# Kernel optimization log

Measured on AMD Instinct MI355X. Metric: run time of the kernel, lower is better.

The kernel has to match this reference:

```python
import jax, jax.numpy as jnp
import numpy as np
from jax import lax

E = 8          # num_experts
K = 2          # top-k
TASKS = 8
GATE_DIM = 16
# (in, expand, out, kernel, stride) per MoE stage
STAGES = [(3, 32, 16, 7, 2), (16, 64, 32, 3, 1), (32, 128, 64, 3, 2), (64, 256, 64, 3, 1), (64, 128, 32, 3, 1)]
DN = ('NCHW', 'OIHW', 'NCHW')


def _pw(x, w):
    return lax.conv_general_dilated(x, w, (1, 1), 'VALID', dimension_numbers=DN)


def _dw(x, w, s):
    p = w.shape[-1] // 2
    return lax.conv_general_dilated(x, w, (s, s), [(p, p), (p, p)], dimension_numbers=DN, feature_group_count=x.shape[1])


def _gn(x, scale, bias):
    # GroupNorm with num_groups = C // 4, eps = 1e-5 (torch default)
    B, C, H, W = x.shape
    G = C // 4
    xr = x.reshape(B, G, -1)
    m = xr.mean(-1, keepdims=True)
    v = xr.var(-1, keepdims=True)
    xn = ((xr - m) * lax.rsqrt(v + 1e-5)).reshape(B, C, H, W)
    return xn * scale[None, :, None, None] + bias[None, :, None, None]


def _dsc(x, p, stride):
    # DSCBlock: pw-conv -> GN -> SiLU -> dw-conv -> GN -> SiLU -> pw-conv -> GN
    w1, s1, b1, w2, s2, b2, w3, s3, b3 = p
    x = jax.nn.silu(_gn(_pw(x, w1), s1, b1))
    x = jax.nn.silu(_gn(_dw(x, w2, stride), s2, b2))
    return _gn(_pw(x, w3), s3, b3)


def _moe(gate_input, x, wg, p, stride, task_bh):
    # task-conditioned top-k softmax gating (noisy_gating=False, all aux loss weights 0)
    logits = gate_input @ wg[task_bh]                      # (B, E)
    probs = jax.nn.softmax(logits, axis=-1)
    topv, topi = lax.top_k(probs, K)
    topv = topv / topv.sum(-1, keepdims=True)              # renormalize top-k gates
    Bn = gate_input.shape[0]
    dense = jnp.zeros_like(probs).at[jnp.arange(Bn)[:, None], topi].set(topv)
    eo = jax.vmap(lambda pe: _dsc(x, pe, stride))(p)       # (E, B, C, H, W)
    return jnp.einsum('be,ebchw->bchw', dense, eo)


def _forward(fl, task_bh):
    gi, xi, ppe = fl[0], fl[1], fl[2]
    x = xi
    for i, (_, _, _, _, s) in enumerate(STAGES):
        base = 3 + i * 10
        wg = fl[base]
        p = tuple(fl[base + 1: base + 10])
        x = _moe(gi, x, wg, p, s, task_bh)
    Bn = x.shape[0]
    # patchify: (B,32,20,20) -> unfold(2,4,4).unfold(3,4,4) -> permute -> (B,25,512)
    patches = x.reshape(Bn, 32, 5, 4, 5, 4).transpose(0, 1, 2, 4, 3, 5)  # (B,32,5,5,4,4)
    patches = patches.transpose(0, 2, 3, 4, 5, 1).reshape(Bn, 25, 512)
    return patches + ppe


def setup_inputs():
    key = jax.random.key(0)
    ks = iter(jax.random.split(key, 256))
    B = 64
    d = {}
    d['gate_input'] = jax.random.normal(next(ks), (B, GATE_DIM), jnp.float32)
    d['expert_input'] = jax.random.normal(next(ks), (B, 3, 80, 80), jnp.float32)
    d['patch_pos_embed'] = 0.02 * jax.random.normal(next(ks), (1, 25, 512), jnp.float32)
    for i, (cin, exp, cout, k, s) in enumerate(STAGES, 1):
        d[f's{i}_wg'] = 0.1 * jax.random.normal(next(ks), (TASKS, GATE_DIM, E), jnp.float32)
        d[f's{i}_w1'] = jax.random.normal(next(ks), (E, exp, cin, 1, 1), jnp.float32) / np.sqrt(cin)
        d[f's{i}_g1s'] = 1.0 + 0.1 * jax.random.normal(next(ks), (E, exp), jnp.float32)
        d[f's{i}_g1b'] = 0.1 * jax.random.normal(next(ks), (E, exp), jnp.float32)
        d[f's{i}_w2'] = jax.random.normal(next(ks), (E, exp, 1, k, k), jnp.float32) / k
        d[f's{i}_g2s'] = 1.0 + 0.1 * jax.random.normal(next(ks), (E, exp), jnp.float32)
        d[f's{i}_g2b'] = 0.1 * jax.random.normal(next(ks), (E, exp), jnp.float32)
        d[f's{i}_w3'] = jax.random.normal(next(ks), (E, cout, exp, 1, 1), jnp.float32) / np.sqrt(exp)
        d[f's{i}_g3s'] = 1.0 + 0.1 * jax.random.normal(next(ks), (E, cout), jnp.float32)
        d[f's{i}_g3b'] = 0.1 * jax.random.normal(next(ks), (E, cout), jnp.float32)
    d['task_bh'] = 3
    return d


def reference(gate_input, expert_input, patch_pos_embed, s1_wg, s1_w1, s1_g1s, s1_g1b, s1_w2, s1_g2s, s1_g2b, s1_w3, s1_g3s, s1_g3b, s2_wg, s2_w1, s2_g1s, s2_g1b, s2_w2, s2_g2s, s2_g2b, s2_w3, s2_g3s, s2_g3b, s3_wg, s3_w1, s3_g1s, s3_g1b, s3_w2, s3_g2s, s3_g2b, s3_w3, s3_g3s, s3_g3b, s4_wg, s4_w1, s4_g1s, s4_g1b, s4_w2, s4_g2s, s4_g2b, s4_w3, s4_g3s, s4_g3b, s5_wg, s5_w1, s5_g1s, s5_g1b, s5_w2, s5_g2s, s5_g2b, s5_w3, s5_g3s, s5_g3b, task_bh):
    fl = (gate_input, expert_input, patch_pos_embed,
          s1_wg, s1_w1, s1_g1s, s1_g1b, s1_w2, s1_g2s, s1_g2b, s1_w3, s1_g3s, s1_g3b,
          s2_wg, s2_w1, s2_g1s, s2_g1b, s2_w2, s2_g2s, s2_g2b, s2_w3, s2_g3s, s2_g3b,
          s3_wg, s3_w1, s3_g1s, s3_g1b, s3_w2, s3_g2s, s3_g2b, s3_w3, s3_g3s, s3_g3b,
          s4_wg, s4_w1, s4_g1s, s4_g1b, s4_w2, s4_g2s, s4_g2b, s4_w3, s4_g3s, s4_g3b,
          s5_wg, s5_w1, s5_g1s, s5_g1b, s5_w2, s5_g2s, s5_g2b, s5_w3, s5_g3s, s5_g3b)
    patches = _forward(fl, task_bh)
    loss = jnp.zeros((), patches.dtype)  # all MoE loss weights are 0 in VisionEncoder
    return (patches, loss)
```

## Files before the change

kernel.cpp:

```cpp
#include <hip/hip_runtime.h>
#include <cstddef>

#define TPB 256

typedef __attribute__((ext_vector_type(8))) short short8v;
typedef __attribute__((ext_vector_type(4))) float f32x4;

__device__ __forceinline__ int rfl(int v) { return __builtin_amdgcn_readfirstlane(v); }
__device__ __forceinline__ float rflf(float v) {
    return __int_as_float(__builtin_amdgcn_readfirstlane(__float_as_int(v)));
}

__device__ __forceinline__ unsigned short f2bf(float f) {
    union { float f; unsigned int u; } x{f};
    unsigned int r = x.u + 0x7fffu + ((x.u >> 16) & 1u);
    return (unsigned short)(r >> 16);
}
__device__ __forceinline__ float bf2f(unsigned short u) {
    return __uint_as_float(((unsigned int)u) << 16);
}

template <int N, int NW>
__device__ __forceinline__ void bredN(float* v, float* red) {
    __syncthreads();
    #pragma unroll
    for (int off = 32; off > 0; off >>= 1)
        #pragma unroll
        for (int i = 0; i < N; i++) v[i] += __shfl_down(v[i], off);
    const int lane = threadIdx.x & 63;
    const int wv = threadIdx.x >> 6;
    if (lane == 0)
        #pragma unroll
        for (int i = 0; i < N; i++) red[wv * N + i] = v[i];
    __syncthreads();
    if (threadIdx.x == 0) {
        #pragma unroll
        for (int i = 0; i < N; i++) {
            float s = 0.f;
            #pragma unroll
            for (int w = 0; w < NW; w++) s += red[w * N + i];
            red[i] = s;
        }
    }
    __syncthreads();
    #pragma unroll
    for (int i = 0; i < N; i++) v[i] = red[i];
}

__device__ __forceinline__ float silu_f(float v) {
    return v * __builtin_amdgcn_rcpf(1.f + __expf(-v));
}

struct GatePtrs { const float* wg[5]; };

__global__ void gate_kernel(const float* __restrict__ gi, GatePtrs gp,
                            const int* __restrict__ taskp,
                            int* __restrict__ gidx, float* __restrict__ gw) {
    const int s = blockIdx.x;
    const int b = threadIdx.x;
    const int task = taskp[0];
    const float* wg = gp.wg[s] + (size_t)task * 16 * 8;
    float l[8];
    #pragma unroll
    for (int e = 0; e < 8; e++) l[e] = 0.f;
    for (int d = 0; d < 16; d++) {
        float v = gi[b * 16 + d];
        #pragma unroll
        for (int e = 0; e < 8; e++) l[e] += v * wg[d * 8 + e];
    }
    float mx = l[0];
    #pragma unroll
    for (int e = 1; e < 8; e++) mx = fmaxf(mx, l[e]);
    float p[8]; float sum = 0.f;
    #pragma unroll
    for (int e = 0; e < 8; e++) { p[e] = expf(l[e] - mx); sum += p[e]; }
    int i0 = 0;
    #pragma unroll
    for (int e = 1; e < 8; e++) if (p[e] > p[i0]) i0 = e;
    int i1 = (i0 == 0) ? 1 : 0;
    #pragma unroll
    for (int e = 0; e < 8; e++) if (e != i0 && p[e] > p[i1]) i1 = e;
    const float denom = p[i0] + p[i1];
    const int base = (s * 64 + b) * 2;
    gidx[base] = i0; gidx[base + 1] = i1;
    gw[base] = p[i0] / denom; gw[base + 1] = p[i1] / denom;
}

template <int M, int K, int N, int MT, int NCHK, bool FOLD, bool BIN>
__global__ __launch_bounds__(256) void gemm_bf16(
    const unsigned short* __restrict__ inp, const float* __restrict__ wmat,
    const int* __restrict__ gidx, const float* __restrict__ foldStats,
    const float* __restrict__ foldS, const float* __restrict__ foldB,
    unsigned short* __restrict__ outp, float* __restrict__ stats) {
    constexpr int KITERS = (K + 31) / 32;
    constexpr int IM = (MT == 64) ? 2 : 1;
    constexpr int IN = (MT == 16) ? 1 : 2;
    const int bx = blockIdx.x;
    const int nc = bx % NCHK, mc = bx / NCHK;
    const int b = blockIdx.y, slot = blockIdx.z;
    const int bs = b * 2 + slot;
    const int e = rfl(gidx[b * 2 + slot]);
    const int n0 = nc * 64, m0 = mc * MT;
    const int tid = threadIdx.x;
    const int lane = tid & 63, wv = tid >> 6;
    const int quad = lane >> 4, l15 = lane & 15;

    __shared__ __align__(16) unsigned short wtile[MT * 40];
    __shared__ unsigned int intile[16 * 65];
    __shared__ float sred[(MT / 4) * 2];
    __shared__ float afv[K], bfv[K];

    if (tid < (MT / 4) * 2) sred[tid] = 0.f;
    if constexpr (FOLD) {
        for (int c = tid; c < K; c += 256) {
            const int g = c >> 2;
            const float s1 = foldStats[((size_t)bs * (K / 4) + g) * 2 + 0];
            const float s2 = foldStats[((size_t)bs * (K / 4) + g) * 2 + 1];
            const float mean = s1 / (4.f * N);
            const float var = s2 / (4.f * N) - mean * mean;
            const float inv = rsqrtf(var + 1e-5f);
            const float sc = foldS[e * K + c], bi = foldB[e * K + c];
            afv[c] = inv * sc;
            bfv[c] = bi - mean * inv * sc;
        }
    }

    int mbase, nbase;
    if constexpr (MT == 64) { mbase = (wv & 1) * 32; nbase = (wv >> 1) * 32; }
    else if constexpr (MT == 32) { mbase = (wv & 1) * 16; nbase = (wv >> 1) * 32; }
    else { mbase = 0; nbase = wv * 16; }

    f32x4 acc[IM][IN];
    #pragma unroll
    for (int im = 0; im < IM; im++)
        #pragma unroll
        for (int in = 0; in < IN; in++)
            #pragma unroll
            for (int r = 0; r < 4; r++) acc[im][in][r] = 0.f;

    const unsigned short* ib = inp + (size_t)(BIN ? b : bs) * K * N;
    const float* wbase = wmat + (size_t)e * M * K;

    for (int k0 = 0; k0 < KITERS * 32; k0 += 32) {
        __syncthreads();
        for (int i = tid; i < MT * 32; i += 256) {
            const int m = i >> 5, kk = i & 31;
            const float v = (k0 + kk < K) ? wbase[(size_t)(m0 + m) * K + k0 + kk] : 0.f;
            wtile[m * 40 + kk] = f2bf(v);
        }
        {
            const int kp = tid >> 4, nq = tid & 15;
            const int k = k0 + kp * 2;
            const int n = n0 + nq * 4;
            unsigned short u0[4] = {0, 0, 0, 0}, u1[4] = {0, 0, 0, 0};
            const bool nv = (n < N);
            if (nv && k < K) {
                const ushort4 t = *(const ushort4*)(ib + (size_t)k * N + n);
                u0[0] = t.x; u0[1] = t.y; u0[2] = t.z; u0[3] = t.w;
            }
            if (nv && k + 1 < K) {
                const ushort4 t = *(const ushort4*)(ib + (size_t)(k + 1) * N + n);
                u1[0] = t.x; u1[1] = t.y; u1[2] = t.z; u1[3] = t.w;
            }
            #pragma unroll
            for (int t = 0; t < 4; t++) {
                float f0, f1;
                if constexpr (FOLD) {
                    f0 = (nv && k < K) ? silu_f(afv[k] * bf2f(u0[t]) + bfv[k]) : 0.f;
                    f1 = (nv && k + 1 < K) ? silu_f(afv[k + 1] * bf2f(u1[t]) + bfv[k + 1]) : 0.f;
                } else {
                    f0 = bf2f(u0[t]); f1 = bf2f(u1[t]);
                }
                intile[kp * 65 + nq * 4 + t] =
                    (unsigned int)f2bf(f0) | ((unsigned int)f2bf(f1) << 16);
            }
        }
        __syncthreads();

        short8v afr[IM];
        #pragma unroll
        for (int im = 0; im < IM; im++) {
            const int m = mbase + im * 16 + l15;
            afr[im] = *(const short8v*)&wtile[m * 40 + quad * 8];
        }
        #pragma unroll
        for (int in = 0; in < IN; in++) {
            union { unsigned int u[4]; short8v s; } bu;
            const int col = nbase + in * 16 + l15;
            #pragma unroll
            for (int i = 0; i < 4; i++) bu.u[i] = intile[(quad * 4 + i) * 65 + col];
            #pragma unroll
            for (int im = 0; im < IM; im++)
                acc[im][in] = __builtin_amdgcn_mfma_f32_16x16x32_bf16(
                    afr[im], bu.s, acc[im][in], 0, 0, 0);
        }
    }

    unsigned short* ob = outp + (size_t)bs * M * N;
    #pragma unroll
    for (int im = 0; im < IM; im++) {
        #pragma unroll
        for (int in = 0; in < IN; in++) {
            const int n = n0 + nbase + in * 16 + l15;
            float s1 = 0.f, s2 = 0.f;
            #pragma unroll
            for (int r = 0; r < 4; r++) {
                const float a = acc[im][in][r];
                s1 += a; s2 += a * a;
            }
            if (n < N) {
                #pragma unroll
                for (int r = 0; r < 4; r++) {
                    const int m = m0 + mbase + im * 16 + quad * 4 + r;
                    ob[(size_t)m * N + n] = f2bf(acc[im][in][r]);
                }
            }
            #pragma unroll
            for (int off = 8; off > 0; off >>= 1) {
                s1 += __shfl_down(s1, off, 16);
                s2 += __shfl_down(s2, off, 16);
            }
            if (l15 == 0) {
                const int gl = (mbase + im * 16) / 4 + quad;
                atomicAdd(&sred[gl * 2 + 0], s1);
                atomicAdd(&sred[gl * 2 + 1], s2);
            }
        }
    }
    __syncthreads();
    for (int i = tid; i < MT / 4; i += 256) {
        float* sp = stats + (((size_t)bs * (M / 4) + mc * (MT / 4) + i) * NCHK + nc) * 2;
        sp[0] = sred[i * 2]; sp[1] = sred[i * 2 + 1];
    }
}

template <int CEXP, int H, int W, int NCH, int TPBk, int NCHK1>
__global__ __launch_bounds__(TPBk) void dw_k(
    const unsigned short* __restrict__ raw1, const float* __restrict__ stats1,
    const float* __restrict__ g1s, const float* __restrict__ g1b,
    const float* __restrict__ w2, const int* __restrict__ gidx,
    unsigned short* __restrict__ act2raw, float* __restrict__ stats2) {
    constexpr int HW = H * W, HP = H + 2, WPL = W + 3;
    constexpr int NPV = HW / 4, NG = NCH / 4, NW = TPBk / 64;
    constexpr int Qc = HW / 4, QT = NCH * Qc, QI = (QT + TPBk - 1) / TPBk;
    constexpr int G1 = CEXP / 4;
    const int gch = blockIdx.x, b = blockIdx.y, slot = blockIdx.z;
    const int bs = b * 2 + slot;
    const int tid = threadIdx.x;
    const int e = rfl(gidx[b * 2 + slot]);
    const int cb0 = gch * NCH;

    __shared__ float buf1[NCH * HP * WPL];
    __shared__ float w2s[NCH * 9];
    __shared__ float afl[NCH], bfl[NCH];
    __shared__ float red[2 * NG * NW];

    for (int i = tid; i < NCH * HP * WPL; i += TPBk) buf1[i] = 0.f;
    if (tid < NCH * 9) w2s[tid] = w2[((size_t)e * CEXP + cb0) * 9 + tid];
    if (tid < NCH) {
        const int c = cb0 + tid, g = c >> 2;
        float s1 = 0.f, s2 = 0.f;
        for (int i = 0; i < NCHK1; i++) {
            s1 += stats1[(((size_t)bs * G1 + g) * NCHK1 + i) * 2 + 0];
            s2 += stats1[(((size_t)bs * G1 + g) * NCHK1 + i) * 2 + 1];
        }
        const float mean = s1 / (4.f * HW);
        const float var = s2 / (4.f * HW) - mean * mean;
        const float inv = rsqrtf(var + 1e-5f);
        const float sc = g1s[e * CEXP + c], bi = g1b[e * CEXP + c];
        afl[tid] = inv * sc; bfl[tid] = bi - mean * inv * sc;
    }
    __syncthreads();

    const unsigned short* rb = raw1 + (size_t)bs * CEXP * HW + (size_t)cb0 * HW;
    for (int i = tid; i < NCH * NPV; i += TPBk) {
        const int c = i / NPV, pv = i - c * NPV;
        const int p4 = pv * 4, ph = p4 / W, pwb = p4 - ph * W;
        const ushort4 u = *(const ushort4*)(rb + (size_t)c * HW + p4);
        const float a = afl[c], bb = bfl[c];
        float* bp = &buf1[(c * HP + ph + 1) * WPL + pwb + 1];
        bp[0] = silu_f(a * bf2f(u.x) + bb);
        bp[1] = silu_f(a * bf2f(u.y) + bb);
        bp[2] = silu_f(a * bf2f(u.z) + bb);
        bp[3] = silu_f(a * bf2f(u.w) + bb);
    }
    __syncthreads();

    float st2[2 * NG];
    #pragma unroll
    for (int i = 0; i < 2 * NG; i++) st2[i] = 0.f;
    unsigned short* ao = act2raw + (size_t)bs * CEXP * HW + (size_t)cb0 * HW;
    #pragma unroll
    for (int qi = 0; qi < QI; qi++) {
        const int q = tid + qi * TPBk;
        if (QI * TPBk == QT || q < QT) {
            const int c = q / Qc, qq = q - c * Qc;
            const int oh = qq % H, owb = (qq / H) * 4;
            float o[4] = {0.f, 0.f, 0.f, 0.f};
            #pragma unroll
            for (int kh = 0; kh < 3; kh++) {
                const int base = (c * HP + oh + kh) * WPL + owb;
                float r[6];
                #pragma unroll
                for (int i = 0; i < 6; i++) r[i] = buf1[base + i];
                const float wa = w2s[c * 9 + kh * 3 + 0];
                const float wb = w2s[c * 9 + kh * 3 + 1];
                const float wcc = w2s[c * 9 + kh * 3 + 2];
                #pragma unroll
                for (int t = 0; t < 4; t++)
                    o[t] += wa * r[t] + wb * r[t + 1] + wcc * r[t + 2];
            }
            ushort4 ov = {f2bf(o[0]), f2bf(o[1]), f2bf(o[2]), f2bf(o[3])};
            *(ushort4*)(ao + c * HW + oh * W + owb) = ov;
            #pragma unroll
            for (int t = 0; t < 4; t++) {
                if constexpr (NG == 1) { st2[0] += o[t]; st2[1] += o[t] * o[t]; }
                else {
                    const bool gs = (c >= 4);
                    float a0 = gs ? 0.f : o[t], a1 = gs ? o[t] : 0.f;
                    st2[0] += a0; st2[1] += a0 * a0;
                    st2[2] += a1; st2[3] += a1 * a1;
                }
            }
        }
    }
    bredN<2 * NG, NW>(st2, red);
    if (tid == 0) {
        #pragma unroll
        for (int g = 0; g < NG; g++) {
            stats2[((size_t)bs * G1 + cb0 / 4 + g) * 2 + 0] = st2[g * 2];
            stats2[((size_t)bs * G1 + cb0 / 4 + g) * 2 + 1] = st2[g * 2 + 1];
        }
    }
}

__global__ __launch_bounds__(256) void s1_stats(
    const float* __restrict__ xin, const float* __restrict__ w1,
    const int* __restrict__ gidx, float* __restrict__ stats1) {
    const int g = blockIdx.x, b = blockIdx.y, slot = blockIdx.z;
    const int tid = threadIdx.x;
    const int e = rfl(gidx[b * 2 + slot]);
    __shared__ float red[8];
    const float* xb = xin + (size_t)b * 3 * 6400;
    const float* w1e = w1 + ((size_t)e * 32 + g * 4) * 3;
    float wr[4][3];
    #pragma unroll
    for (int c = 0; c < 4; c++)
        #pragma unroll
        for (int k = 0; k < 3; k++) wr[c][k] = rflf(w1e[c * 3 + k]);
    float s[2] = {0.f, 0.f};
    #pragma unroll
    for (int j = 0; j < 7; j++) {
        const int i = j * 256 + tid;
        if (i < 1600) {
            const int p4 = i * 4;
            const float4 v0 = *(const float4*)(xb + p4);
            const float4 v1 = *(const float4*)(xb + 6400 + p4);
            const float4 v2 = *(const float4*)(xb + 12800 + p4);
            const float a0[4] = {v0.x, v0.y, v0.z, v0.w};
            const float a1[4] = {v1.x, v1.y, v1.z, v1.w};
            const float a2[4] = {v2.x, v2.y, v2.z, v2.w};
            #pragma unroll
            for (int t = 0; t < 4; t++)
                #pragma unroll
                for (int c = 0; c < 4; c++) {
                    float a = fmaf(wr[c][0], a0[t], fmaf(wr[c][1], a1[t], wr[c][2] * a2[t]));
                    s[0] += a; s[1] += a * a;
                }
        }
    }
    bredN<2, 4>(s, red);
    if (tid == 0) {
        float* sp = stats1 + ((size_t)(b * 2 + slot) * 8 + g) * 2;
        sp[0] = s[0]; sp[1] = s[1];
    }
}

__global__ __launch_bounds__(256) void s1_band(
    const float* __restrict__ xin, const float* __restrict__ w1,
    const float* __restrict__ g1s, const float* __restrict__ g1b,
    const float* __restrict__ w2, const int* __restrict__ gidx,
    const float* __restrict__ stats1,
    float* __restrict__ rawdw, float* __restrict__ stats2) {
    constexpr int NR = 25, RW = 90, EVO = 44;
    const int gb = blockIdx.x;
    const int g = gb >> 2, band = gb & 3;
    const int b = blockIdx.y, slot = blockIdx.z;
    const int tid = threadIdx.x;
    const int e = rfl(gidx[b * 2 + slot]);

    __shared__ float sbuf[4 * NR * RW];
    __shared__ float w2s[196];
    __shared__ float red[8];

    for (int i = tid; i < 4 * NR * RW; i += 256) sbuf[i] = 0.f;
    if (tid < 196) w2s[tid] = w2[((size_t)e * 32 + g * 4) * 49 + tid];

    const float* sp = stats1 + ((size_t)(b * 2 + slot) * 8 + g) * 2;
    const float s1v = rflf(sp[0]), s2v = rflf(sp[1]);
    const float mean = s1v / 25600.f;
    const float var = s2v / 25600.f - mean * mean;
    const float inv = rsqrtf(var + 1e-5f);

    const float* xb = xin + (size_t)b * 3 * 6400;
    const float* w1e = w1 + ((size_t)e * 32 + g * 4) * 3;
    float wr[4][3], sc1r[4], bi1r[4];
    #pragma unroll
    for (int c = 0; c < 4; c++) {
        #pragma unroll
        for (int k = 0; k < 3; k++) wr[c][k] = rflf(w1e[c * 3 + k]);
        sc1r[c] = rflf(g1s[e * 32 + g * 4 + c]);
        bi1r[c] = rflf(g1b[e * 32 + g * 4 + c]);
    }
    const int oh0 = band * 10;
    const int rlo = 2 * oh0 - 3;
    __syncthreads();

    for (int ii = tid; ii < 500; ii += 256) {
        const int p4 = ii * 4;
        const int l = p4 / 80, pw = p4 - l * 80;
        const int r = rlo + l;
        if (r >= 0 && r < 80) {
            const float4 v0 = *(const float4*)(xb + r * 80 + pw);
            const float4 v1 = *(const float4*)(xb + 6400 + r * 80 + pw);
            const float4 v2 = *(const float4*)(xb + 12800 + r * 80 + pw);
            const float a0[4] = {v0.x, v0.y, v0.z, v0.w};
            const float a1[4] = {v1.x, v1.y, v1.z, v1.w};
            const float a2[4] = {v2.x, v2.y, v2.z, v2.w};
            #pragma unroll
            for (int c = 0; c < 4; c++) {
                #pragma unroll
                for (int t = 0; t < 4; t++) {
                    float a = fmaf(wr[c][0], a0[t], fmaf(wr[c][1], a1[t], wr[c][2] * a2[t]));
                    float v = silu_f((a - mean) * inv * sc1r[c] + bi1r[c]);
                    const int cc = pw + t + 3;
                    const int sl = (cc & 1) ? EVO + (cc >> 1) : (cc >> 1);
                    sbuf[(c * NR + l) * RW + sl] = v;
                }
            }
        }
    }
    __syncthreads();

    float st2[2] = {0.f, 0.f};
    float* rw = rawdw + (size_t)(b * 2 + slot) * 32 * 1600 + (size_t)g * 4 * 1600;
    #pragma unroll
    for (int qi = 0; qi < 2; qi++) {
        const int q = tid + qi * 256;
        if (q < 400) {
            const int c = q / 100;
            const int rem = q - c * 100;
            const int ohl = rem / 10, owb = (rem - ohl * 10) * 4;
            float o[4] = {0.f, 0.f, 0.f, 0.f};
            #pragma unroll
            for (int kh = 0; kh < 7; kh++) {
                const int base = (c * NR + 2 * ohl + kh) * RW;
                const float2 e01 = *(const float2*)&sbuf[base + owb];
                const float2 e23 = *(const float2*)&sbuf[base + owb + 2];
                const float2 e45 = *(const float2*)&sbuf[base + owb + 4];
                const float e6 = sbuf[base + owb + 6];
                const float2 q01 = *(const float2*)&sbuf[base + EVO + owb];
                const float2 q23 = *(const float2*)&sbuf[base + EVO + owb + 2];
                const float2 q45 = *(const float2*)&sbuf[base + EVO + owb + 4];
                const float evr[7] = {e01.x, e01.y, e23.x, e23.y, e45.x, e45.y, e6};
                const float odr[6] = {q01.x, q01.y, q23.x, q23.y, q45.x, q45.y};
                const float w0 = w2s[c * 49 + kh * 7 + 0];
                const float w1v = w2s[c * 49 + kh * 7 + 1];
                const float w2v = w2s[c * 49 + kh * 7 + 2];
                const float w3 = w2s[c * 49 + kh * 7 + 3];
                const float w4 = w2s[c * 49 + kh * 7 + 4];
                const float w5 = w2s[c * 49 + kh * 7 + 5];
                const float w6 = w2s[c * 49 + kh * 7 + 6];
                #pragma unroll
                for (int t = 0; t < 4; t++)
                    o[t] += w0 * evr[t] + w1v * odr[t] + w2v * evr[t + 1]
                          + w3 * odr[t + 1] + w4 * evr[t + 2] + w5 * odr[t + 2]
                          + w6 * evr[t + 3];
            }
            const int oh = oh0 + ohl;
            float4 ov = {o[0], o[1], o[2], o[3]};
            *(float4*)(rw + c * 1600 + oh * 40 + owb) = ov;
            #pragma unroll
            for (int t = 0; t < 4; t++) { st2[0] += o[t]; st2[1] += o[t] * o[t]; }
        }
    }
    bredN<2, 4>(st2, red);
    if (tid == 0) {
        float* s2p = stats2 + (((size_t)(b * 2 + slot) * 8 + g) * 4 + band) * 2;
        s2p[0] = st2[0]; s2p[1] = st2[1];
    }
}

__global__ __launch_bounds__(256) void s1_norm(
    const float* __restrict__ rawdw, const float* __restrict__ stats2,
    const float* __restrict__ g2s, const float* __restrict__ g2b,
    const int* __restrict__ gidx, unsigned short* __restrict__ act2) {
    const int g = blockIdx.x, b = blockIdx.y, slot = blockIdx.z;
    const int tid = threadIdx.x;
    const int e = rfl(gidx[b * 2 + slot]);
    const float* sp = stats2 + ((size_t)(b * 2 + slot) * 8 + g) * 8;
    const float s1 = rflf(sp[0]) + rflf(sp[2]) + rflf(sp[4]) + rflf(sp[6]);
    const float s2 = rflf(sp[1]) + rflf(sp[3]) + rflf(sp[5]) + rflf(sp[7]);
    const float mean2 = s1 / 6400.f;
    const float var2 = s2 / 6400.f - mean2 * mean2;
    const float inv2 = rsqrtf(var2 + 1e-5f);
    const float* rb = rawdw + (size_t)(b * 2 + slot) * 32 * 1600 + (size_t)g * 4 * 1600;
    unsigned short* ao = act2 + ((size_t)(b * 2 + slot) * 32 + g * 4) * 1600;
    #pragma unroll
    for (int c = 0; c < 4; c++) {
        const float sc = rflf(g2s[e * 32 + g * 4 + c]);
        const float bi = rflf(g2b[e * 32 + g * 4 + c]);
        #pragma unroll
        for (int qi = 0; qi < 2; qi++) {
            const int i = tid + qi * 256;
            if (i < 400) {
                const float4 v = *(const float4*)(rb + c * 1600 + i * 4);
                ushort4 ov;
                ov.x = f2bf(silu_f((v.x - mean2) * inv2 * sc + bi));
                ov.y = f2bf(silu_f((v.y - mean2) * inv2 * sc + bi));
                ov.z = f2bf(silu_f((v.z - mean2) * inv2 * sc + bi));
                ov.w = f2bf(silu_f((v.w - mean2) * inv2 * sc + bi));
                *(ushort4*)(ao + c * 1600 + i * 4) = ov;
            }
        }
    }
}

template <int CIN, int CEXP, int KS, int STRIDE, int H, int W, int HO, int WO,
          int NCH, int TPBk>
__global__ __launch_bounds__(TPBk) void dsc_ab_v2(
    const unsigned short* __restrict__ xin, const float* __restrict__ w1,
    const float* __restrict__ g1s, const float* __restrict__ g1b,
    const float* __restrict__ w2,
    const float* __restrict__ g2s, const float* __restrict__ g2b,
    const int* __restrict__ gidx, unsigned short* __restrict__ act2) {
    constexpr int HW = H * W, HWO = HO * WO;
    constexpr int HP = H + 2, WPL = W + 3, EVW = (W + 2) / 2;
    constexpr int NPV = HW / 4;
    constexpr int JN = (NPV + TPBk - 1) / TPBk;
    constexpr int NW = TPBk / 64;
    constexpr int NG = NCH / 4;
    constexpr int Qc = HWO / 4;
    constexpr int QT = NCH * Qc;
    constexpr int QI = (QT + TPBk - 1) / TPBk;
    constexpr int KK = KS * KS;
    const int gch = blockIdx.x, b = blockIdx.y, slot = blockIdx.z;
    const int tid = threadIdx.x;
    const int e = rfl(gidx[b * 2 + slot]);
    const int cb0 = gch * NCH;

    __shared__ float buf1[NCH * HP * WPL];
    __shared__ float w2s[NCH * KK];
    __shared__ float sc2s[NCH], bi2s[NCH];
    __shared__ float red[2 * NG * NW];

    for (int i = tid; i < NCH * HP * WPL; i += TPBk) buf1[i] = 0.f;
    for (int i = tid; i < NCH * KK; i += TPBk) {
        int c = i / KK, k = i - c * KK;
        w2s[i] = w2[((size_t)e * CEXP + cb0 + c) * KK + k];
    }
    if (tid < NCH) {
        sc2s[tid] = g2s[e * CEXP + cb0 + tid];
        bi2s[tid] = g2b[e * CEXP + cb0 + tid];
    }

    const unsigned short* xb = xin + (size_t)b * CIN * HW;
    const float* w1e = w1 + ((size_t)e * CEXP + cb0) * CIN;

    float acc[NCH][JN][4];
    #pragma unroll
    for (int c = 0; c < NCH; c++)
        #pragma unroll
        for (int j = 0; j < JN; j++)
            #pragma unroll
            for (int t = 0; t < 4; t++) acc[c][j][t] = 0.f;

    for (int cb = 0; cb < CIN; cb += 4) {
        float wr[NCH][4];
        #pragma unroll
        for (int c = 0; c < NCH; c++)
            #pragma unroll
            for (int k = 0; k < 4; k++) wr[c][k] = rflf(w1e[c * CIN + cb + k]);
        #pragma unroll
        for (int j = 0; j < JN; j++) {
            const int pv = tid + j * TPBk;
            if (JN * TPBk == NPV || pv < NPV) {
                #pragma unroll
                for (int k = 0; k < 4; k++) {
                    const ushort4 v4 = *(const ushort4*)(xb + (cb + k) * HW + pv * 4);
                    const float va[4] = {bf2f(v4.x), bf2f(v4.y), bf2f(v4.z), bf2f(v4.w)};
                    #pragma unroll
                    for (int c = 0; c < NCH; c++)
                        #pragma unroll
                        for (int t = 0; t < 4; t++)
                            acc[c][j][t] = fmaf(wr[c][k], va[t], acc[c][j][t]);
                }
            }
        }
    }
    float st[2 * NG];
    #pragma unroll
    for (int i = 0; i < 2 * NG; i++) st[i] = 0.f;
    #pragma unroll
    for (int c = 0; c < NCH; c++) {
        const int gs = (c >> 2) * 2;
        #pragma unroll
        for (int j = 0; j < JN; j++)
            #pragma unroll
            for (int t = 0; t < 4; t++) {
                float a = acc[c][j][t];
                st[gs] += a; st[gs + 1] += a * a;
            }
    }
    bredN<2 * NG, NW>(st, red);
    float mg[NG], ig[NG];
    #pragma unroll
    for (int g = 0; g < NG; g++) {
        mg[g] = st[g * 2] / (4.f * HW);
        float var = st[g * 2 + 1] / (4.f * HW) - mg[g] * mg[g];
        ig[g] = rsqrtf(var + 1e-5f);
    }
    float sc1r[NCH], bi1r[NCH];
    #pragma unroll
    for (int c = 0; c < NCH; c++) {
        sc1r[c] = rflf(g1s[e * CEXP + cb0 + c]);
        bi1r[c] = rflf(g1b[e * CEXP + cb0 + c]);
    }
    #pragma unroll
    for (int j = 0; j < JN; j++) {
        const int pv = tid + j * TPBk;
        if (JN * TPBk == NPV || pv < NPV) {
            const int p4 = pv * 4;
            const int ph = p4 / W, pwb = p4 - ph * W;
            #pragma unroll
            for (int c = 0; c < NCH; c++) {
                const int g = (NG == 1) ? 0 : (c >> 2);
// ... 33 lines not shown
                    const float wa = w2s[c * KK + kh * KS + 0];
                    const float wb = w2s[c * KK + kh * KS + 1];
                    const float wcc = w2s[c * KK + kh * KS + 2];
                    #pragma unroll
                    for (int t = 0; t < 4; t++)
                        o[t] += wa * r[t] + wb * r[t + 1] + wcc * r[t + 2];
                }
            } else {
                #pragma unroll
                for (int kh = 0; kh < KS; kh++) {
                    const int base = (c * HP + 2 * oh + kh) * WPL;
                    float ev[5], od[4];
                    #pragma unroll
                    for (int i = 0; i < 5; i++) ev[i] = buf1[base + owb + i];
                    #pragma unroll
                    for (int i = 0; i < 4; i++) od[i] = buf1[base + EVW + owb + i];
                    const float wa = w2s[c * KK + kh * KS + 0];
                    const float wb = w2s[c * KK + kh * KS + 1];
                    const float wcc = w2s[c * KK + kh * KS + 2];
                    #pragma unroll
                    for (int t = 0; t < 4; t++)
                        o[t] += wa * ev[t] + wb * od[t] + wcc * ev[t + 1];
                }
            }
            #pragma unroll
            for (int t = 0; t < 4; t++) {
                float a = o[t];
                dacc[qi][t] = a;
                if constexpr (NG == 1) {
                    st2[0] += a; st2[1] += a * a;
                } else {
                    const bool gsel = (c >= 4);
                    float a0 = gsel ? 0.f : a, a1 = gsel ? a : 0.f;
                    st2[0] += a0; st2[1] += a0 * a0;
                    st2[2] += a1; st2[3] += a1 * a1;
                }
            }
        }
    }
    bredN<2 * NG, NW>(st2, red);
    float m2[NG], i2[NG];
    #pragma unroll
    for (int g = 0; g < NG; g++) {
        m2[g] = st2[g * 2] / (4.f * HWO);
        float var = st2[g * 2 + 1] / (4.f * HWO) - m2[g] * m2[g];
        i2[g] = rsqrtf(var + 1e-5f);
    }
    unsigned short* ao = act2 + ((size_t)(b * 2 + slot) * CEXP + cb0) * HWO;
    #pragma unroll
    for (int qi = 0; qi < QI; qi++) {
        const int q = tid + qi * TPBk;
        if (QI * TPBk == QT || q < QT) {
            const int c = q / Qc, qq = q - c * Qc;
            const int oh = qq % HO, owb = (qq / HO) * 4;
            const int g = (NG == 1) ? 0 : ((c >= 4) ? 1 : 0);
            const float sc = sc2s[c], bi = bi2s[c];
            ushort4 ov;
            ov.x = f2bf(silu_f((dacc[qi][0] - m2[g]) * i2[g] * sc + bi));
            ov.y = f2bf(silu_f((dacc[qi][1] - m2[g]) * i2[g] * sc + bi));
            ov.z = f2bf(silu_f((dacc[qi][2] - m2[g]) * i2[g] * sc + bi));
            ov.w = f2bf(silu_f((dacc[qi][3] - m2[g]) * i2[g] * sc + bi));
            *(ushort4*)(ao + c * HWO + oh * WO + owb) = ov;
        }
    }
}

template <int COUT, int HWO, int PXC, bool PATCH>
__global__ __launch_bounds__(256) void pw3_k3m(
    const unsigned short* __restrict__ raw3, const float* __restrict__ statsw,
    const float* __restrict__ g3s, const float* __restrict__ g3b,
    const int* __restrict__ gidx, const float* __restrict__ gw,
    const float* __restrict__ ppe, float* __restrict__ outf,
    unsigned short* __restrict__ outb) {
    constexpr int G = COUT / 4;
    constexpr int Q = HWO / 4;
    const int gg = blockIdx.x, b = blockIdx.y;
    const int tid = threadIdx.x;

    float A[2][4], Bv[2][4];
    #pragma unroll
    for (int slot = 0; slot < 2; slot++) {
        const int e = rfl(gidx[b * 2 + slot]);
        const float wgt = rflf(gw[b * 2 + slot]);
        const float* sp = statsw + ((size_t)(b * 2 + slot) * G + gg) * PXC * 2;
        float s1 = 0.f, s2 = 0.f;
        for (int i = 0; i < PXC; i++) { s1 += rflf(sp[i * 2]); s2 += rflf(sp[i * 2 + 1]); }
        const float mean = s1 / (4.f * HWO);
        const float var = s2 / (4.f * HWO) - mean * mean;
        const float inv = rsqrtf(var + 1e-5f);
        #pragma unroll
        for (int i = 0; i < 4; i++) {
            const int c = gg * 4 + i;
            const float sc = rflf(g3s[e * COUT + c]);
            const float bi = rflf(g3b[e * COUT + c]);
            A[slot][i] = wgt * inv * sc;
            Bv[slot][i] = wgt * (bi - mean * inv * sc);
        }
    }

    #pragma unroll
    for (int i = 0; i < 4; i++) {
        const int c = gg * 4 + i;
        const unsigned short* r0 = raw3 + ((size_t)(b * 2 + 0) * COUT + c) * HWO;
        const unsigned short* r1 = raw3 + ((size_t)(b * 2 + 1) * COUT + c) * HWO;
        for (int q = tid; q < Q; q += 256) {
            const int p4 = q * 4;
            const ushort4 u0 = *(const ushort4*)(r0 + p4);
            const ushort4 u1 = *(const ushort4*)(r1 + p4);
            const float v0[4] = {bf2f(u0.x), bf2f(u0.y), bf2f(u0.z), bf2f(u0.w)};
            const float v1[4] = {bf2f(u1.x), bf2f(u1.y), bf2f(u1.z), bf2f(u1.w)};
            float o[4];
            #pragma unroll
            for (int t = 0; t < 4; t++)
                o[t] = fmaf(A[0][i], v0[t], Bv[0][i]) + fmaf(A[1][i], v1[t], Bv[1][i]);
            if constexpr (!PATCH) {
                ushort4 ov = {f2bf(o[0]), f2bf(o[1]), f2bf(o[2]), f2bf(o[3])};
                *(ushort4*)(outb + ((size_t)b * COUT + c) * HWO + p4) = ov;
            } else {
                const int ph = p4 / 20, pw0 = p4 - ph * 20;
                const int p = (ph >> 2) * 5 + (pw0 >> 2);
                const int dbase = ((ph & 3) * 4) * 32 + c;
                float* op = outf + ((size_t)b * 25 + p) * 512;
                const float* pp = ppe + p * 512;
                #pragma unroll
                for (int jj = 0; jj < 4; jj++)
                    op[dbase + jj * 32] = o[jj] + pp[dbase + jj * 32];
            }
        }
    }
    if (PATCH && gg == 0 && b == 0 && tid == 0) outf[64 * 25 * 512] = 0.f;
}

extern "C" void kernel_launch(void* const* d_in, const int* in_sizes, int n_in,
                              void* d_out, int out_size, void* d_ws, size_t ws_size,
                              hipStream_t stream) {
    const float* gate_input = (const float*)d_in[0];
    const float* expert_input = (const float*)d_in[1];
    const float* ppe = (const float*)d_in[2];
    const int* taskp = (const int*)d_in[53];
    auto in = [&](int s, int k) { return (const float*)d_in[3 + s * 10 + k]; };

    char* ws = (char*)d_ws;
    int* gidx = (int*)ws;
    float* gw = (float*)(ws + 4096);
    size_t off = 8192;
    unsigned short* x0 = (unsigned short*)(ws + off); off += (size_t)8 << 20;
    unsigned short* x1 = (unsigned short*)(ws + off); off += (size_t)8 << 20;
    unsigned short* act2 = (unsigned short*)(ws + off); off += (size_t)27 << 20;
    char* bufA = ws + off; off += (size_t)27 << 20;
    float* stats1 = (float*)(ws + off); off += (size_t)2 << 20;
    float* stats2 = (float*)(ws + off); off += 262144;
    float* stats3 = (float*)(ws + off); off += (size_t)1 << 20;
    float* st1a = (float*)(ws + off); off += 65536;
    float* st1b = (float*)(ws + off);
    float* outp = (float*)d_out;

    GatePtrs gp;
    for (int s = 0; s < 5; s++) gp.wg[s] = in(s, 0);
    gate_kernel<<<5, 64, 0, stream>>>(gate_input, gp, taskp, gidx, gw);

    s1_stats<<<dim3(8, 64, 2), 256, 0, stream>>>(expert_input, in(0, 1),
                                                 gidx + 0 * 128, st1a);
    s1_band<<<dim3(32, 64, 2), 256, 0, stream>>>(
        expert_input, in(0, 1), in(0, 2), in(0, 3), in(0, 4),
        gidx + 0 * 128, st1a, (float*)bufA, st1b);
    s1_norm<<<dim3(8, 64, 2), 256, 0, stream>>>(
        (float*)bufA, st1b, in(0, 5), in(0, 6), gidx + 0 * 128, act2);
    gemm_bf16<16, 32, 1600, 16, 25, false, false><<<dim3(25, 64, 2), 256, 0, stream>>>(
        act2, in(0, 7), gidx + 0 * 128, nullptr, nullptr, nullptr,
        (unsigned short*)bufA, stats3);
    pw3_k3m<16, 1600, 25, false><<<dim3(4, 64), 256, 0, stream>>>(
        (unsigned short*)bufA, stats3, in(0, 8), in(0, 9), gidx + 0 * 128,
        gw + 0 * 128, ppe, nullptr, x0);

    gemm_bf16<64, 16, 1600, 64, 25, false, true><<<dim3(25, 64, 2), 256, 0, stream>>>(
        x0, in(1, 1), gidx + 1 * 128, nullptr, nullptr, nullptr,
        (unsigned short*)bufA, stats1);
    dw_k<64, 40, 40, 4, 256, 25><<<dim3(16, 64, 2), 256, 0, stream>>>(
        (unsigned short*)bufA, stats1, in(1, 2), in(1, 3), in(1, 4),
        gidx + 1 * 128, act2, stats2);
    gemm_bf16<32, 64, 1600, 32, 25, true, false><<<dim3(25, 64, 2), 256, 0, stream>>>(
        act2, in(1, 7), gidx + 1 * 128, stats2, in(1, 5), in(1, 6),
        (unsigned short*)bufA, stats3);
    pw3_k3m<32, 1600, 25, false><<<dim3(8, 64), 256, 0, stream>>>(
        (unsigned short*)bufA, stats3, in(1, 8), in(1, 9), gidx + 1 * 128,
        gw + 1 * 128, ppe, nullptr, x1);

    dsc_ab_v2<32, 128, 3, 2, 40, 40, 20, 20, 4, 256><<<dim3(32, 64, 2), 256, 0, stream>>>(
        x1, in(2, 1), in(2, 2), in(2, 3), in(2, 4), in(2, 5), in(2, 6),
        gidx + 2 * 128, act2);
    gemm_bf16<64, 128, 400, 64, 7, false, false><<<dim3(7, 64, 2), 256, 0, stream>>>(
        act2, in(2, 7), gidx + 2 * 128, nullptr, nullptr, nullptr,
        (unsigned short*)bufA, stats3);
    pw3_k3m<64, 400, 7, false><<<dim3(16, 64), 256, 0, stream>>>(
        (unsigned short*)bufA, stats3, in(2, 8), in(2, 9), gidx + 2 * 128,
        gw + 2 * 128, ppe, nullptr, x0);

    gemm_bf16<256, 64, 400, 64, 7, false, true><<<dim3(28, 64, 2), 256, 0, stream>>>(
        x0, in(3, 1), gidx + 3 * 128, nullptr, nullptr, nullptr,
        (unsigned short*)bufA, stats1);
    dw_k<256, 20, 20, 8, 128, 7><<<dim3(32, 64, 2), 128, 0, stream>>>(
        (unsigned short*)bufA, stats1, in(3, 2), in(3, 3), in(3, 4),
        gidx + 3 * 128, act2, stats2);
    gemm_bf16<64, 256, 400, 64, 7, true, false><<<dim3(7, 64, 2), 256, 0, stream>>>(
        act2, in(3, 7), gidx + 3 * 128, stats2, in(3, 5), in(3, 6),
        (unsigned short*)bufA, stats3);
    pw3_k3m<64, 400, 7, false><<<dim3(16, 64), 256, 0, stream>>>(
        (unsigned short*)bufA, stats3, in(3, 8), in(3, 9), gidx + 3 * 128,
        gw + 3 * 128, ppe, nullptr, x1);

    gemm_bf16<128, 64, 400, 64, 7, false, true><<<dim3(14, 64, 2), 256, 0, stream>>>(
        x1, in(4, 1), gidx + 4 * 128, nullptr, nullptr, nullptr,
        (unsigned short*)bufA, stats1);
    dw_k<128, 20, 20, 8, 128, 7><<<dim3(16, 64, 2), 128, 0, stream>>>(
        (unsigned short*)bufA, stats1, in(4, 2), in(4, 3), in(4, 4),
        gidx + 4 * 128, act2, stats2);
    gemm_bf16<32, 128, 400, 32, 7, true, false><<<dim3(7, 64, 2), 256, 0, stream>>>(
        act2, in(4, 7), gidx + 4 * 128, stats2, in(4, 5), in(4, 6),
        (unsigned short*)bufA, stats3);
    pw3_k3m<32, 400, 7, true><<<dim3(8, 64), 256, 0, stream>>>(
        (unsigned short*)bufA, stats3, in(4, 8), in(4, 9), gidx + 4 * 128,
        gw + 4 * 128, ppe, outp, nullptr);
}
```

Before: 523.9 us.

## Pre-split GEMM weights into bf16 hi/lo pairs and use bf16 LDS in stage-1 dwconv

A new prep kernel converts all pointwise weights to bf16 high and low parts once per call. The GEMMs load these pre-converted halves instead of converting fp32 in the loop, and issue two MFMAs per tile to recover near-fp32 weight precision. The stage-1 depthwise band kernel now stores activations as bf16 in shared memory and computes one output per thread instead of four. dw_k and the GEMM gain channel-offset parameters, which are set to identity values. The changes trade extra MFMA work, an extra launch and lower activation precision for lower conversion and LDS cost.

```diff
diff --git a/kernel.cpp b/kernel.cpp
--- a/kernel.cpp
+++ b/kernel.cpp
@@ -52,6 +52,21 @@
 }
 
 struct GatePtrs { const float* wg[5]; };
+struct WSrcs { const float* p[9]; };
+
+__global__ __launch_bounds__(256) void wprep(WSrcs wsrc,
+                                             unsigned short* __restrict__ whi,
+                                             unsigned short* __restrict__ wlo) {
+    const int sizes[9] = {4096, 8192, 16384, 32768, 65536, 131072, 131072, 65536, 32768};
+    int idx = blockIdx.x * 256 + threadIdx.x;
+    if (idx >= 487424) return;
+    int rem = idx, s = 0;
+    while (s < 8 && rem >= sizes[s]) { rem -= sizes[s]; s++; }
+    const float v = wsrc.p[s][rem];
+    const unsigned short h = f2bf(v);
+    whi[idx] = h;
+    wlo[idx] = f2bf(v - bf2f(h));
+}
 
 __global__ void gate_kernel(const float* __restrict__ gi, GatePtrs gp,
                             const int* __restrict__ taskp,
@@ -88,10 +103,12 @@
 
 template <int M, int K, int N, int MT, int NCHK, bool FOLD, bool BIN>
 __global__ __launch_bounds__(256) void gemm_bf16(
-    const unsigned short* __restrict__ inp, const float* __restrict__ wmat,
+    const unsigned short* __restrict__ inp,
+    const unsigned short* __restrict__ whi, const unsigned short* __restrict__ wlo,
     const int* __restrict__ gidx, const float* __restrict__ foldStats,
     const float* __restrict__ foldS, const float* __restrict__ foldB,
-    unsigned short* __restrict__ outp, float* __restrict__ stats) {
+    unsigned short* __restrict__ outp, float* __restrict__ stats,
+    int mfull, int moff) {
     constexpr int KITERS = (K + 31) / 32;
     constexpr int IM = (MT == 64) ? 2 : 1;
     constexpr int IN = (MT == 16) ? 1 : 2;
@@ -105,7 +122,8 @@
     const int lane = tid & 63, wv = tid >> 6;
     const int quad = lane >> 4, l15 = lane & 15;
 
-    __shared__ __align__(16) unsigned short wtile[MT * 40];
+    __shared__ __align__(16) unsigned short wtileH[MT * 40];
+    __shared__ __align__(16) unsigned short wtileL[MT * 40];
     __shared__ unsigned int intile[16 * 65];
     __shared__ float sred[(MT / 4) * 2];
     __shared__ float afv[K], bfv[K];
@@ -139,14 +157,17 @@
             for (int r = 0; r < 4; r++) acc[im][in][r] = 0.f;
 
     const unsigned short* ib = inp + (size_t)(BIN ? b : bs) * K * N;
-    const float* wbase = wmat + (size_t)e * M * K;
+    const unsigned short* wbH = whi + ((size_t)e * mfull + moff) * K;
+    const unsigned short* wbL = wlo + ((size_t)e * mfull + moff) * K;
 
     for (int k0 = 0; k0 < KITERS * 32; k0 += 32) {
         __syncthreads();
         for (int i = tid; i < MT * 32; i += 256) {
             const int m = i >> 5, kk = i & 31;
-            const float v = (k0 + kk < K) ? wbase[(size_t)(m0 + m) * K + k0 + kk] : 0.f;
-            wtile[m * 40 + kk] = f2bf(v);
+            const bool ok = (k0 + kk < K);
+            const size_t src = (size_t)(m0 + m) * K + k0 + kk;
+            wtileH[m * 40 + kk] = ok ? wbH[src] : (unsigned short)0;
+            wtileL[m * 40 + kk] = ok ? wbL[src] : (unsigned short)0;
         }
         {
             const int kp = tid >> 4, nq = tid & 15;
@@ -177,11 +198,12 @@
         }
         __syncthreads();
 
-        short8v afr[IM];
+        short8v afrH[IM], afrL[IM];
         #pragma unroll
         for (int im = 0; im < IM; im++) {
             const int m = mbase + im * 16 + l15;
-            afr[im] = *(const short8v*)&wtile[m * 40 + quad * 8];
+            afrH[im] = *(const short8v*)&wtileH[m * 40 + quad * 8];
+            afrL[im] = *(const short8v*)&wtileL[m * 40 + quad * 8];
         }
         #pragma unroll
         for (int in = 0; in < IN; in++) {
@@ -190,9 +212,12 @@
             #pragma unroll
             for (int i = 0; i < 4; i++) bu.u[i] = intile[(quad * 4 + i) * 65 + col];
             #pragma unroll
-            for (int im = 0; im < IM; im++)
+            for (int im = 0; im < IM; im++) {
                 acc[im][in] = __builtin_amdgcn_mfma_f32_16x16x32_bf16(
-                    afr[im], bu.s, acc[im][in], 0, 0, 0);
+                    afrH[im], bu.s, acc[im][in], 0, 0, 0);
+                acc[im][in] = __builtin_amdgcn_mfma_f32_16x16x32_bf16(
+                    afrL[im], bu.s, acc[im][in], 0, 0, 0);
+            }
         }
     }
 
@@ -229,26 +254,28 @@
     }
     __syncthreads();
     for (int i = tid; i < MT / 4; i += 256) {
-        float* sp = stats + (((size_t)bs * (M / 4) + mc * (MT / 4) + i) * NCHK + nc) * 2;
+        float* sp = stats + (((size_t)bs * (mfull / 4) + moff / 4 + mc * (MT / 4) + i)
+                             * NCHK + nc) * 2;
         sp[0] = sred[i * 2]; sp[1] = sred[i * 2 + 1];
     }
 }
 
-template <int CEXP, int H, int W, int NCH, int TPBk, int NCHK1>
+template <int CLOC, int CFULL, int H, int W, int NCH, int TPBk, int NCHK1>
 __global__ __launch_bounds__(TPBk) void dw_k(
     const unsigned short* __restrict__ raw1, const float* __restrict__ stats1,
     const float* __restrict__ g1s, const float* __restrict__ g1b,
     const float* __restrict__ w2, const int* __restrict__ gidx,
-    unsigned short* __restrict__ act2raw, float* __restrict__ stats2) {
+    unsigned short* __restrict__ act2raw, float* __restrict__ stats2, int coff) {
     constexpr int HW = H * W, HP = H + 2, WPL = W + 3;
     constexpr int NPV = HW / 4, NG = NCH / 4, NW = TPBk / 64;
     constexpr int Qc = HW / 4, QT = NCH * Qc, QI = (QT + TPBk - 1) / TPBk;
-    constexpr int G1 = CEXP / 4;
+    constexpr int G1 = CFULL / 4;
     const int gch = blockIdx.x, b = blockIdx.y, slot = blockIdx.z;
     const int bs = b * 2 + slot;
     const int tid = threadIdx.x;
     const int e = rfl(gidx[b * 2 + slot]);
     const int cb0 = gch * NCH;
+    const int cg0 = coff + cb0;
 
     __shared__ float buf1[NCH * HP * WPL];
     __shared__ float w2s[NCH * 9];
@@ -256,9 +283,9 @@
     __shared__ float red[2 * NG * NW];
 
     for (int i = tid; i < NCH * HP * WPL; i += TPBk) buf1[i] = 0.f;
-    if (tid < NCH * 9) w2s[tid] = w2[((size_t)e * CEXP + cb0) * 9 + tid];
+    if (tid < NCH * 9) w2s[tid] = w2[((size_t)e * CFULL + cg0) * 9 + tid];
     if (tid < NCH) {
-        const int c = cb0 + tid, g = c >> 2;
+        const int g = (cg0 + tid) >> 2;
         float s1 = 0.f, s2 = 0.f;
         for (int i = 0; i < NCHK1; i++) {
             s1 += stats1[(((size_t)bs * G1 + g) * NCHK1 + i) * 2 + 0];
@@ -267,12 +294,12 @@
         const float mean = s1 / (4.f * HW);
         const float var = s2 / (4.f * HW) - mean * mean;
         const float inv = rsqrtf(var + 1e-5f);
-        const float sc = g1s[e * CEXP + c], bi = g1b[e * CEXP + c];
+        const float sc = g1s[e * CFULL + cg0 + tid], bi = g1b[e * CFULL + cg0 + tid];
         afl[tid] = inv * sc; bfl[tid] = bi - mean * inv * sc;
     }
     __syncthreads();
 
-    const unsigned short* rb = raw1 + (size_t)bs * CEXP * HW + (size_t)cb0 * HW;
+    const unsigned short* rb = raw1 + (size_t)bs * CLOC * HW + (size_t)cb0 * HW;
     for (int i = tid; i < NCH * NPV; i += TPBk) {
         const int c = i / NPV, pv = i - c * NPV;
         const int p4 = pv * 4, ph = p4 / W, pwb = p4 - ph * W;
@@ -289,7 +316,7 @@
     float st2[2 * NG];
     #pragma unroll
     for (int i = 0; i < 2 * NG; i++) st2[i] = 0.f;
-    unsigned short* ao = act2raw + (size_t)bs * CEXP * HW + (size_t)cb0 * HW;
+    unsigned short* ao = act2raw + (size_t)bs * CFULL * HW + (size_t)cg0 * HW;
     #pragma unroll
     for (int qi = 0; qi < QI; qi++) {
         const int q = tid + qi * TPBk;
@@ -328,8 +355,8 @@
     if (tid == 0) {
         #pragma unroll
         for (int g = 0; g < NG; g++) {
-            stats2[((size_t)bs * G1 + cb0 / 4 + g) * 2 + 0] = st2[g * 2];
-            stats2[((size_t)bs * G1 + cb0 / 4 + g) * 2 + 1] = st2[g * 2 + 1];
+            stats2[((size_t)bs * G1 + cg0 / 4 + g) * 2 + 0] = st2[g * 2];
+            stats2[((size_t)bs * G1 + cg0 / 4 + g) * 2 + 1] = st2[g * 2 + 1];
         }
     }
 }
@@ -382,18 +409,18 @@
     const float* __restrict__ w2, const int* __restrict__ gidx,
     const float* __restrict__ stats1,
     float* __restrict__ rawdw, float* __restrict__ stats2) {
-    constexpr int NR = 25, RW = 90, EVO = 44;
+    constexpr int NR = 25, RW32 = 43;
     const int gb = blockIdx.x;
     const int g = gb >> 2, band = gb & 3;
     const int b = blockIdx.y, slot = blockIdx.z;
     const int tid = threadIdx.x;
     const int e = rfl(gidx[b * 2 + slot]);
 
-    __shared__ float sbuf[4 * NR * RW];
+    __shared__ unsigned int sbuf[4 * NR * RW32];
     __shared__ float w2s[196];
     __shared__ float red[8];
 
-    for (int i = tid; i < 4 * NR * RW; i += 256) sbuf[i] = 0.f;
+    for (int i = tid; i < 4 * NR * RW32; i += 256) sbuf[i] = 0u;
     if (tid < 196) w2s[tid] = w2[((size_t)e * 32 + g * 4) * 49 + tid];
 
     const float* sp = stats1 + ((size_t)(b * 2 + slot) * 8 + g) * 2;
@@ -416,6 +443,7 @@
     const int rlo = 2 * oh0 - 3;
     __syncthreads();
 
+    unsigned short* sb16 = (unsigned short*)sbuf;
     for (int ii = tid; ii < 500; ii += 256) {
         const int p4 = ii * 4;
         const int l = p4 / 80, pw = p4 - l * 80;
@@ -429,13 +457,11 @@
             const float a2[4] = {v2.x, v2.y, v2.z, v2.w};
             #pragma unroll
             for (int c = 0; c < 4; c++) {
+                unsigned short* row16 = sb16 + ((c * NR + l) * RW32) * 2 + pw + 3;
                 #pragma unroll
                 for (int t = 0; t < 4; t++) {
                     float a = fmaf(wr[c][0], a0[t], fmaf(wr[c][1], a1[t], wr[c][2] * a2[t]));
-                    float v = silu_f((a - mean) * inv * sc1r[c] + bi1r[c]);
-                    const int cc = pw + t + 3;
-                    const int sl = (cc & 1) ? EVO + (cc >> 1) : (cc >> 1);
-                    sbuf[(c * NR + l) * RW + sl] = v;
+                    row16[t] = f2bf(silu_f((a - mean) * inv * sc1r[c] + bi1r[c]));
                 }
             }
         }
@@ -445,43 +471,27 @@
     float st2[2] = {0.f, 0.f};
     float* rw = rawdw + (size_t)(b * 2 + slot) * 32 * 1600 + (size_t)g * 4 * 1600;
     #pragma unroll
-    for (int qi = 0; qi < 2; qi++) {
+    for (int qi = 0; qi < 7; qi++) {
         const int q = tid + qi * 256;
-        if (q < 400) {
-            const int c = q / 100;
-            const int rem = q - c * 100;
-            const int ohl = rem / 10, owb = (rem - ohl * 10) * 4;
-            float o[4] = {0.f, 0.f, 0.f, 0.f};
+        if (q < 1600) {
+            const int c = q / 400, rem = q - c * 400;
+            const int ow = rem % 40, ohl = rem / 40;
+            float o = 0.f;
             #pragma unroll
             for (int kh = 0; kh < 7; kh++) {
-                const int base = (c * NR + 2 * ohl + kh) * RW;
-                const float2 e01 = *(const float2*)&sbuf[base + owb];
-                const float2 e23 = *(const float2*)&sbuf[base + owb + 2];
-                const float2 e45 = *(const float2*)&sbuf[base + owb + 4];
-                const float e6 = sbuf[base + owb + 6];
-                const float2 q01 = *(const float2*)&sbuf[base + EVO + owb];
-                const float2 q23 = *(const float2*)&sbuf[base + EVO + owb + 2];
-                const float2 q45 = *(const float2*)&sbuf[base + EVO + owb + 4];
-                const float evr[7] = {e01.x, e01.y, e23.x, e23.y, e45.x, e45.y, e6};
-                const float odr[6] = {q01.x, q01.y, q23.x, q23.y, q45.x, q45.y};
-                const float w0 = w2s[c * 49 + kh * 7 + 0];
-                const float w1v = w2s[c * 49 + kh * 7 + 1];
-                const float w2v = w2s[c * 49 + kh * 7 + 2];
-                const float w3 = w2s[c * 49 + kh * 7 + 3];
-                const float w4 = w2s[c * 49 + kh * 7 + 4];
-                const float w5 = w2s[c * 49 + kh * 7 + 5];
-                const float w6 = w2s[c * 49 + kh * 7 + 6];
-                #pragma unroll
-                for (int t = 0; t < 4; t++)
-                    o[t] += w0 * evr[t] + w1v * odr[t] + w2v * evr[t + 1]
-                          + w3 * odr[t + 1] + w4 * evr[t + 2] + w5 * odr[t + 2]
-                          + w6 * evr[t + 3];
-            }
-            const int oh = oh0 + ohl;
-            float4 ov = {o[0], o[1], o[2], o[3]};
-            *(float4*)(rw + c * 1600 + oh * 40 + owb) = ov;
-            #pragma unroll
-            for (int t = 0; t < 4; t++) { st2[0] += o[t]; st2[1] += o[t] * o[t]; }
+                const unsigned int* rp = &sbuf[(c * NR + 2 * ohl + kh) * RW32 + ow];
+                const unsigned int d0 = rp[0], d1 = rp[1], d2 = rp[2], d3 = rp[3];
+                const float* wk = &w2s[c * 49 + kh * 7];
+                o += wk[0] * __uint_as_float(d0 << 16)
+                   + wk[1] * __uint_as_float(d0 & 0xffff0000u)
+                   + wk[2] * __uint_as_float(d1 << 16)
+                   + wk[3] * __uint_as_float(d1 & 0xffff0000u)
+                   + wk[4] * __uint_as_float(d2 << 16)
+                   + wk[5] * __uint_as_float(d2 & 0xffff0000u)
+                   + wk[6] * __uint_as_float(d3 << 16);
+            }
+            rw[c * 1600 + (oh0 + ohl) * 40 + ow] = o;
+            st2[0] += o; st2[1] += o * o;
         }
     }
     bredN<2, 4>(st2, red);
@@ -821,12 +831,21 @@
     float* stats2 = (float*)(ws + off); off += 262144;
     float* stats3 = (float*)(ws + off); off += (size_t)1 << 20;
     float* st1a = (float*)(ws + off); off += 65536;
-    float* st1b = (float*)(ws + off);
+    float* st1b = (float*)(ws + off); off += 65536;
+    unsigned short* whi = (unsigned short*)(ws + off); off += 487424 * 2;
+    unsigned short* wlo = (unsigned short*)(ws + off); off += 487424 * 2;
     float* outp = (float*)d_out;
+    unsigned short* bufA16 = (unsigned short*)bufA;
+
+    WSrcs wsrc;
+    wsrc.p[0] = in(0, 7); wsrc.p[1] = in(1, 1); wsrc.p[2] = in(1, 7);
+    wsrc.p[3] = in(2, 1); wsrc.p[4] = in(2, 7); wsrc.p[5] = in(3, 1);
+    wsrc.p[6] = in(3, 7); wsrc.p[7] = in(4, 1); wsrc.p[8] = in(4, 7);
 
     GatePtrs gp;
     for (int s = 0; s < 5; s++) gp.wg[s] = in(s, 0);
     gate_kernel<<<5, 64, 0, stream>>>(gate_input, gp, taskp, gidx, gw);
+    wprep<<<(487424 + 255) / 256, 256, 0, stream>>>(wsrc, whi, wlo);
 
     s1_stats<<<dim3(8, 64, 2), 256, 0, stream>>>(expert_input, in(0, 1),
                                                  gidx + 0 * 128, st1a);
@@ -836,58 +855,58 @@
     s1_norm<<<dim3(8, 64, 2), 256, 0, stream>>>(
         (float*)bufA, st1b, in(0, 5), in(0, 6), gidx + 0 * 128, act2);
     gemm_bf16<16, 32, 1600, 16, 25, false, false><<<dim3(25, 64, 2), 256, 0, stream>>>(
-        act2, in(0, 7), gidx + 0 * 128, nullptr, nullptr, nullptr,
-        (unsigned short*)bufA, stats3);
+        act2, whi + 0, wlo + 0, gidx + 0 * 128, nullptr, nullptr, nullptr,
+        bufA16, stats3, 16, 0);
     pw3_k3m<16, 1600, 25, false><<<dim3(4, 64), 256, 0, stream>>>(
-        (unsigned short*)bufA, stats3, in(0, 8), in(0, 9), gidx + 0 * 128,
+        bufA16, stats3, in(0, 8), in(0, 9), gidx + 0 * 128,
         gw + 0 * 128, ppe, nullptr, x0);
 
     gemm_bf16<64, 16, 1600, 64, 25, false, true><<<dim3(25, 64, 2), 256, 0, stream>>>(
-        x0, in(1, 1), gidx + 1 * 128, nullptr, nullptr, nullptr,
-        (unsigned short*)bufA, stats1);
-    dw_k<64, 40, 40, 4, 256, 25><<<dim3(16, 64, 2), 256, 0, stream>>>(
-        (unsigned short*)bufA, stats1, in(1, 2), in(1, 3), in(1, 4),
-        gidx + 1 * 128, act2, stats2);
+        x0, whi + 4096, wlo + 4096, gidx + 1 * 128, nullptr, nullptr, nullptr,
+        bufA16, stats1, 64, 0);
+    dw_k<64, 64, 40, 40, 4, 256, 25><<<dim3(16, 64, 2), 256, 0, stream>>>(
+        bufA16, stats1, in(1, 2), in(1, 3), in(1, 4),
+        gidx + 1 * 128, act2, stats2, 0);
     gemm_bf16<32, 64, 1600, 32, 25, true, false><<<dim3(25, 64, 2), 256, 0, stream>>>(
-        act2, in(1, 7), gidx + 1 * 128, stats2, in(1, 5), in(1, 6),
-        (unsigned short*)bufA, stats3);
+        act2, whi + 12288, wlo + 12288, gidx + 1 * 128, stats2, in(1, 5), in(1, 6),
+        bufA16, stats3, 32, 0);
     pw3_k3m<32, 1600, 25, false><<<dim3(8, 64), 256, 0, stream>>>(
-        (unsigned short*)bufA, stats3, in(1, 8), in(1, 9), gidx + 1 * 128,
+        bufA16, stats3, in(1, 8), in(1, 9), gidx + 1 * 128,
         gw + 1 * 128, ppe, nullptr, x1);
 
     dsc_ab_v2<32, 128, 3, 2, 40, 40, 20, 20, 4, 256><<<dim3(32, 64, 2), 256, 0, stream>>>(
         x1, in(2, 1), in(2, 2), in(2, 3), in(2, 4), in(2, 5), in(2, 6),
         gidx + 2 * 128, act2);
     gemm_bf16<64, 128, 400, 64, 7, false, false><<<dim3(7, 64, 2), 256, 0, stream>>>(
-        act2, in(2, 7), gidx + 2 * 128, nullptr, nullptr, nullptr,
-        (unsigned short*)bufA, stats3);
+        act2, whi + 61440, wlo + 61440, gidx + 2 * 128, nullptr, nullptr, nullptr,
+        bufA16, stats3, 64, 0);
     pw3_k3m<64, 400, 7, false><<<dim3(16, 64), 256, 0, stream>>>(
-        (unsigned short*)bufA, stats3, in(2, 8), in(2, 9), gidx + 2 * 128,
+        bufA16, stats3, in(2, 8), in(2, 9), gidx + 2 * 128,
         gw + 2 * 128, ppe, nullptr, x0);
 
     gemm_bf16<256, 64, 400, 64, 7, false, true><<<dim3(28, 64, 2), 256, 0, stream>>>(
-        x0, in(3, 1), gidx + 3 * 128, nullptr, nullptr, nullptr,
-        (unsigned short*)bufA, stats1);
-    dw_k<256, 20, 20, 8, 128, 7><<<dim3(32, 64, 2), 128, 0, stream>>>(
-        (unsigned short*)bufA, stats1, in(3, 2), in(3, 3), in(3, 4),
-        gidx + 3 * 128, act2, stats2);
+        x0, whi + 126976, wlo + 126976, gidx + 3 * 128, nullptr, nullptr, nullptr,
+        bufA16, stats1, 256, 0);
+    dw_k<256, 256, 20, 20, 8, 128, 7><<<dim3(32, 64, 2), 128, 0, stream>>>(
+        bufA16, stats1, in(3, 2), in(3, 3), in(3, 4),
+        gidx + 3 * 128, act2, stats2, 0);
     gemm_bf16<64, 256, 400, 64, 7, true, false><<<dim3(7, 64, 2), 256, 0, stream>>>(
-        act2, in(3, 7), gidx + 3 * 128, stats2, in(3, 5), in(3, 6),
-        (unsigned short*)bufA, stats3);
+        act2, whi + 258048, wlo + 258048, gidx + 3 * 128, stats2, in(3, 5), in(3, 6),
+        bufA16, stats3, 64, 0);
     pw3_k3m<64, 400, 7, false><<<dim3(16, 64), 256, 0, stream>>>(
-        (unsigned short*)bufA, stats3, in(3, 8), in(3, 9), gidx + 3 * 128,
+        bufA16, stats3, in(3, 8), in(3, 9), gidx + 3 * 128,
         gw + 3 * 128, ppe, nullptr, x1);
 
     gemm_bf16<128, 64, 400, 64, 7, false, true><<<dim3(14, 64, 2), 256, 0, stream>>>(
-        x1, in(4, 1), gidx + 4 * 128, nullptr, nullptr, nullptr,
-        (unsigned short*)bufA, stats1);
-    dw_k<128, 20, 20, 8, 128, 7><<<dim3(16, 64, 2), 128, 0, stream>>>(
-        (unsigned short*)bufA, stats1, in(4, 2), in(4, 3), in(4, 4),
-        gidx + 4 * 128, act2, stats2);
+        x1, whi + 389120, wlo + 389120, gidx + 4 * 128, nullptr, nullptr, nullptr,
+        bufA16, stats1, 128, 0);
+    dw_k<128, 128, 20, 20, 8, 128, 7><<<dim3(16, 64, 2), 128, 0, stream>>>(
+        bufA16, stats1, in(4, 2), in(4, 3), in(4, 4),
+        gidx + 4 * 128, act2, stats2, 0);
     gemm_bf16<32, 128, 400, 32, 7, true, false><<<dim3(7, 64, 2), 256, 0, stream>>>(
-        act2, in(4, 7), gidx + 4 * 128, stats2, in(4, 5), in(4, 6),
-        (unsigned short*)bufA, stats3);
+        act2, whi + 454656, wlo + 454656, gidx + 4 * 128, stats2, in(4, 5), in(4, 6),
+        bufA16, stats3, 32, 0);
     pw3_k3m<32, 400, 7, true><<<dim3(8, 64), 256, 0, stream>>>(
-        (unsigned short*)bufA, stats3, in(4, 8), in(4, 9), gidx + 4 * 128,
+        bufA16, stats3, in(4, 8), in(4, 9), gidx + 4 * 128,
         gw + 4 * 128, ppe, outp, nullptr);
 }
```

Measured after the change: 550.5 us. 5.1% more time.
